# Optimization experiments

Measured on AMD Instinct MI355X. Metric: run time of the kernel, lower is better.

Reference implementation:

```python
import jax, jax.numpy as jnp
import numpy as np

ANNEAL = 0.01  # sigmoid temperature from __init__


def _tsigmoid(x, temp):
    # temperature-controlled sigmoid with the original exponent clamp
    e = jnp.clip(-x / temp, -50.0, 50.0)
    return 1.0 / (1.0 + jnp.exp(e))


def setup_inputs() -> dict:
    key = jax.random.key(0)
    k1, k2 = jax.random.split(key)
    embeddings = jax.random.normal(k1, (384, 512), dtype=jnp.float32)
    labels = jax.random.randint(k2, (384, 40), 0, 2).astype(jnp.int32)
    return {"embeddings": embeddings, "labels": labels}


def reference(embeddings, labels):
    B = embeddings.shape[0]
    # F.normalize(dim=-1) with eps=1e-12
    norm = jnp.maximum(jnp.linalg.norm(embeddings, axis=-1, keepdims=True), 1e-12)
    x = embeddings / norm
    sim = x @ x.T                                   # [B,B] affinity

    # sg[q,j,k] = sigmoid((sim[q,k] - sim[q,j]) / T); diag over (j,k) is exactly 0.5
    sg = _tsigmoid(sim[:, None, :] - sim[:, :, None], ANNEAL)  # [B,B,B]

    # rank over ALL items, excluding k==j (mask = 1-eye): subtract the 0.5 diagonal
    rk_all = 1.0 + sg.sum(-1) - 0.5                 # [B,B]

    pos = labels.astype(sim.dtype).T                # [L,B] binary positive masks
    cnt = pos.sum(-1)                               # [L] positives per label

    # rank among positives of label l: sum over positive k (k != j)
    rk_pos = 1.0 + jnp.einsum('qjk,lk->lqj', sg, pos) - 0.5 * pos[:, None, :]  # [L,B,B]

    # sum over positive (q,j) pairs (including q==j, as in index_select x2)
    pair = pos[:, :, None] * pos[:, None, :]        # [L,B,B]
    s = jnp.sum(pair * (rk_pos / rk_all[None]), axis=(1, 2))  # [L]

    valid = cnt > 1.0                               # labels with >1 positive
    ap = jnp.where(valid, s / jnp.maximum(cnt, 1.0) / B, 0.0)
    n_valid = jnp.maximum(jnp.sum(valid.astype(ap.dtype)), 1.0)
    return jnp.sum((1.0 - ap) * valid.astype(ap.dtype)) / n_valid
```

## Files before the change

kernel.cpp:

```cpp
#include <hip/hip_runtime.h>
#include <hip/hip_bf16.h>
#include <math.h>

#define BN 384
#define DD 512
#define LN 40
#define CLOG 144.26950408889634f

typedef __attribute__((ext_vector_type(8))) short short8;
typedef __attribute__((ext_vector_type(4))) float f32x4;
typedef unsigned short u16;

static __device__ __forceinline__ short bfbits(float f) {
    __hip_bfloat16 h = __float2bfloat16(f);
    return __builtin_bit_cast(short, h);
}

__global__ __launch_bounds__(64) void k_norm(const float* __restrict__ emb,
                                             u16* __restrict__ xh,
                                             u16* __restrict__ xl) {
    int r = blockIdx.x;
    int lane = threadIdx.x;
    const float* row = emb + (size_t)r * DD;
    f32x4 v0 = *(const f32x4*)(row + lane * 8);
    f32x4 v1 = *(const f32x4*)(row + lane * 8 + 4);
    float ss = 0.f;
#pragma unroll
    for (int e = 0; e < 4; ++e) { ss = fmaf(v0[e], v0[e], ss); ss = fmaf(v1[e], v1[e], ss); }
#pragma unroll
    for (int off = 32; off; off >>= 1) ss += __shfl_xor(ss, off);
    float inv = 1.0f / fmaxf(sqrtf(ss), 1e-12f);
    short8 hv, lv;
#pragma unroll
    for (int e = 0; e < 8; ++e) {
        float v = (e < 4 ? v0[e] : v1[e - 4]) * inv;
        __hip_bfloat16 hb = __float2bfloat16(v);
        float hf = __bfloat162float(hb);
        hv[e] = __builtin_bit_cast(short, hb);
        lv[e] = bfbits(v - hf);
    }
    *(short8*)(xh + (size_t)r * DD + lane * 8) = hv;
    *(short8*)(xl + (size_t)r * DD + lane * 8) = lv;
}

__global__ __launch_bounds__(256) void k_meta(const int* __restrict__ labels,
                                              float* __restrict__ w,
                                              float* __restrict__ term0,
                                              u16* __restrict__ pfrag) {
    __shared__ int part[240];
    __shared__ float cnt_s[LN];
    __shared__ float nv_s;
    int tid = threadIdx.x;
    if (tid < 240) {
        int l = tid % LN, seg = tid / LN;
        int c = 0;
        for (int k = seg * 64; k < seg * 64 + 64; ++k) c += labels[k * LN + l];
        part[tid] = c;
    }
    __syncthreads();
    if (tid < LN) {
        int c = 0;
#pragma unroll
        for (int s = 0; s < 6; ++s) c += part[s * LN + tid];
        cnt_s[tid] = (float)c;
    }
    __syncthreads();
    if (tid == 0) {
        float nv = 0.f;
        for (int l = 0; l < LN; ++l) nv += (cnt_s[l] > 1.0f) ? 1.f : 0.f;
        term0[0] = (nv > 0.f) ? 1.0f : 0.0f;
        nv_s = fmaxf(nv, 1.0f);
    }
    __syncthreads();
    if (tid < 48)
        w[tid] = (tid < LN && cnt_s[tid] > 1.0f)
                     ? 1.0f / (cnt_s[tid] * (float)BN * nv_s) : 0.0f;
    for (int u = tid; u < 12 * 3 * 64; u += 256) {
        int ks = u / 192, r = u % 192;
        int lt = r >> 6, ln = r & 63;
        int kb = ks * 32 + ((ln >> 4) << 3);
        short8 vals;
#pragma unroll
        for (int e = 0; e < 8; ++e) {
            int k = kb + e;
            int l = lt * 16 + (ln & 15);
            short bv = 0;
            if (l < LN) bv = labels[k * LN + l] ? (short)0x3F80 : (short)0;
            else if (l == LN) bv = (short)0x3F80;
            vals[e] = bv;
        }
        *(short8*)(pfrag + (size_t)u * 8) = vals;
    }
}

__global__ __launch_bounds__(256) void k_sim(const u16* __restrict__ xh,
                                             const u16* __restrict__ xl,
                                             float* __restrict__ sim) {
    int lane = threadIdx.x & 63;
    int wv = threadIdx.x >> 6;
    int i0 = blockIdx.y * 64 + wv * 16;
    int j0 = blockIdx.x * 64;
    f32x4 acc[4];
#pragma unroll
    for (int jt = 0; jt < 4; ++jt) acc[jt] = (f32x4){0.f, 0.f, 0.f, 0.f};
    int r_i = i0 + (lane & 15);
    for (int ks = 0; ks < DD / 32; ++ks) {
        int kb = ks * 32 + ((lane >> 4) << 3);
        short8 ah = *(const short8*)(xh + (size_t)r_i * DD + kb);
        short8 al = *(const short8*)(xl + (size_t)r_i * DD + kb);
#pragma unroll
        for (int jt = 0; jt < 4; ++jt) {
            int r_j = j0 + jt * 16 + (lane & 15);
            short8 bh = *(const short8*)(xh + (size_t)r_j * DD + kb);
            short8 bl = *(const short8*)(xl + (size_t)r_j * DD + kb);
            acc[jt] = __builtin_amdgcn_mfma_f32_16x16x32_bf16(ah, bh, acc[jt], 0, 0, 0);
            acc[jt] = __builtin_amdgcn_mfma_f32_16x16x32_bf16(ah, bl, acc[jt], 0, 0, 0);
            acc[jt] = __builtin_amdgcn_mfma_f32_16x16x32_bf16(al, bh, acc[jt], 0, 0, 0);
        }
    }
    int rbase = i0 + ((lane >> 4) << 2);
#pragma unroll
    for (int jt = 0; jt < 4; ++jt)
#pragma unroll
        for (int rg = 0; rg < 4; ++rg)
            sim[(size_t)(rbase + rg) * BN + j0 + jt * 16 + (lane & 15)] = acc[jt][rg];
}

__global__ __launch_bounds__(256) void k_main(const float* __restrict__ sim,
                                              const int* __restrict__ labels,
                                              const float* __restrict__ w,
                                              const u16* __restrict__ pfrag,
                                              float* __restrict__ partials) {
    __shared__ float a_lds[BN];
    __shared__ float F_lds[BN];
    __shared__ float wql[48];
    __shared__ float red[16];
    __shared__ float m_sh;
    __shared__ float wpart[4];
    int tid = threadIdx.x;
    int bid = blockIdx.x;
    int q = bid >> 1;
    int lane = tid & 63;
    int wv = tid >> 6;

    float mx = -3.0e38f, mn = 3.0e38f;
    for (int i = tid; i < BN; i += 256) {
        float a = sim[(size_t)q * BN + i] * CLOG;
        a_lds[i] = a;
        mx = fmaxf(mx, a); mn = fminf(mn, a);
    }
#pragma unroll
    for (int off = 32; off; off >>= 1) {
        mx = fmaxf(mx, __shfl_xor(mx, off));
        mn = fminf(mn, __shfl_xor(mn, off));
    }
    if (lane == 0) { red[wv] = mx; red[8 + wv] = mn; }
    __syncthreads();
    if (tid == 0) {
        float M = fmaxf(fmaxf(red[0], red[1]), fmaxf(red[2], red[3]));
        float N = fminf(fminf(red[8], red[9]), fminf(red[10], red[11]));
        m_sh = 0.5f * (M + N);
    }
    if (tid < 48) wql[tid] = (tid < LN) ? w[tid] * (float)labels[q * LN + tid] : 0.0f;
    __syncthreads();
    float m = m_sh;
    for (int i = tid; i < BN; i += 256) {
        float d = fminf(fmaxf(m - a_lds[i], -126.f), 126.f);
        F_lds[i] = __builtin_amdgcn_exp2f(d);
    }
    __syncthreads();

    int jbase = (bid & 1) * 192 + wv * 48;
    float E[3];
#pragma unroll
    for (int t = 0; t < 3; ++t) {
        float aj = a_lds[jbase + t * 16 + (lane & 15)];
        E[t] = __builtin_amdgcn_exp2f(fminf(fmaxf(aj - m, -126.f), 126.f));
    }

    f32x4 acc[3][3];
#pragma unroll
    for (int t = 0; t < 3; ++t)
#pragma unroll
        for (int lt = 0; lt < 3; ++lt) acc[t][lt] = (f32x4){0.f, 0.f, 0.f, 0.f};

    int kg = (lane >> 4) << 3;
    for (int ks = 0; ks < 12; ++ks) {
        const u16* pb = pfrag + ((size_t)(ks * 3) * 64 + lane) * 8;
        short8 bf0 = *(const short8*)(pb);
        short8 bf1 = *(const short8*)(pb + 64 * 8);
        short8 bf2 = *(const short8*)(pb + 128 * 8);
        f32x4 fa = *(const f32x4*)&F_lds[ks * 32 + kg];
        f32x4 fb = *(const f32x4*)&F_lds[ks * 32 + kg + 4];
#pragma unroll
        for (int t = 0; t < 3; ++t) {
            float e = E[t];
            short8 af;
#pragma unroll
            for (int u = 0; u < 4; ++u) {
                float p0 = fmaf(e, fa[u], 1.0f);
                float p1 = fmaf(e, fb[u], 1.0f);
                af[u] = bfbits(__builtin_amdgcn_rcpf(p0));
                af[u + 4] = bfbits(__builtin_amdgcn_rcpf(p1));
            }
            acc[t][0] = __builtin_amdgcn_mfma_f32_16x16x32_bf16(af, bf0, acc[t][0], 0, 0, 0);
            acc[t][1] = __builtin_amdgcn_mfma_f32_16x16x32_bf16(af, bf1, acc[t][1], 0, 0, 0);
            acc[t][2] = __builtin_amdgcn_mfma_f32_16x16x32_bf16(af, bf2, acc[t][2], 0, 0, 0);
        }
    }

    float part = 0.f;
#pragma unroll
    for (int t = 0; t < 3; ++t) {
#pragma unroll
        for (int rg = 0; rg < 4; ++rg) {
            int j = jbase + t * 16 + ((lane >> 4) << 2) + rg;
            float av = __shfl(acc[t][2][rg], (lane & 48) | 8);
            float W = __builtin_amdgcn_rcpf(0.5f + av);
            float sv = 0.f;
#pragma unroll
            for (int lt = 0; lt < 3; ++lt) {
                int l = lt * 16 + (lane & 15);
                float pj = (l < LN) ? (float)labels[j * LN + l] : 0.f;
                sv = fmaf(wql[l] * pj, 0.5f + acc[t][lt][rg], sv);
            }
            part = fmaf(W, sv, part);
        }
    }
#pragma unroll
    for (int off = 32; off; off >>= 1) part += __shfl_xor(part, off);
    if (lane == 0) wpart[wv] = part;
    __syncthreads();
    if (tid == 0) partials[bid] = (wpart[0] + wpart[1]) + (wpart[2] + wpart[3]);
}

__global__ __launch_bounds__(64) void k_final(const float* __restrict__ partials,
                                              const float* __restrict__ term0,
                                              float* __restrict__ out) {
    int lane = threadIdx.x;
    float s = 0.f;
    for (int i = lane; i < 768; i += 64) s += partials[i];
#pragma unroll
    for (int off = 32; off; off >>= 1) s += __shfl_xor(s, off);
    if (lane == 0) out[0] = term0[0] - s;
}

extern "C" void kernel_launch(void* const* d_in, const int* in_sizes, int n_in,
                              void* d_out, int out_size, void* d_ws, size_t ws_size,
                              hipStream_t stream) {
    const float* emb = (const float*)d_in[0];
    const int* labels = (const int*)d_in[1];
    float* out = (float*)d_out;

    char* ws = (char*)d_ws;
    u16* xh      = (u16*)(ws);
    u16* xl      = (u16*)(ws + 393216);
    float* sim   = (float*)(ws + 786432);
    u16* pfrag   = (u16*)(ws + 1376256);
    float* w     = (float*)(ws + 1413120);
    float* term0 = (float*)(ws + 1413312);
    float* parts = (float*)(ws + 1413376);

    k_norm<<<dim3(BN), dim3(64), 0, stream>>>(emb, xh, xl);
    k_meta<<<dim3(1), dim3(256), 0, stream>>>(labels, w, term0, pfrag);
    k_sim<<<dim3(6, 6), dim3(256), 0, stream>>>(xh, xl, sim);
    k_main<<<dim3(BN * 2), dim3(256), 0, stream>>>(sim, labels, w, pfrag, parts);
    k_final<<<dim3(1), dim3(64), 0, stream>>>(parts, term0, out);
}
```

Before: 59.35 us.

## Fuse all stages into one cooperative persistent kernel with grid syncs

Replaces the five separate launches (normalize, label metadata, similarity GEMM, main rank pass, final reduce) with a single cooperative kernel. Stages are separated by grid-wide barriers and work is split across waves and blocks with grid-stride loops. The similarity GEMM is re-tiled to one 16x16 tile per wave, which raises parallelism but drops the reuse of the A fragment across four column tiles. This removes launch gaps and the serial single-block meta kernel, at the cost of grid-sync overhead, an occupancy query on the host for every call, and a limit of 3 blocks per CU.

```diff
diff --git a/kernel.cpp b/kernel.cpp
--- a/kernel.cpp
+++ b/kernel.cpp
@@ -1,6 +1,9 @@
 #include <hip/hip_runtime.h>
 #include <hip/hip_bf16.h>
+#include <hip/hip_cooperative_groups.h>
 #include <math.h>
+
+namespace cg = cooperative_groups;
 
 #define BN 384
 #define DD 512
@@ -16,233 +19,225 @@
     return __builtin_bit_cast(short, h);
 }
 
-__global__ __launch_bounds__(64) void k_norm(const float* __restrict__ emb,
-                                             u16* __restrict__ xh,
-                                             u16* __restrict__ xl) {
-    int r = blockIdx.x;
-    int lane = threadIdx.x;
-    const float* row = emb + (size_t)r * DD;
-    f32x4 v0 = *(const f32x4*)(row + lane * 8);
-    f32x4 v1 = *(const f32x4*)(row + lane * 8 + 4);
-    float ss = 0.f;
-#pragma unroll
-    for (int e = 0; e < 4; ++e) { ss = fmaf(v0[e], v0[e], ss); ss = fmaf(v1[e], v1[e], ss); }
-#pragma unroll
-    for (int off = 32; off; off >>= 1) ss += __shfl_xor(ss, off);
-    float inv = 1.0f / fmaxf(sqrtf(ss), 1e-12f);
-    short8 hv, lv;
-#pragma unroll
-    for (int e = 0; e < 8; ++e) {
-        float v = (e < 4 ? v0[e] : v1[e - 4]) * inv;
-        __hip_bfloat16 hb = __float2bfloat16(v);
-        float hf = __bfloat162float(hb);
-        hv[e] = __builtin_bit_cast(short, hb);
-        lv[e] = bfbits(v - hf);
-    }
-    *(short8*)(xh + (size_t)r * DD + lane * 8) = hv;
-    *(short8*)(xl + (size_t)r * DD + lane * 8) = lv;
-}
-
-__global__ __launch_bounds__(256) void k_meta(const int* __restrict__ labels,
-                                              float* __restrict__ w,
-                                              float* __restrict__ term0,
-                                              u16* __restrict__ pfrag) {
-    __shared__ int part[240];
-    __shared__ float cnt_s[LN];
-    __shared__ float nv_s;
+__global__ __launch_bounds__(256, 3) void k_fused(const float* __restrict__ emb,
+                                                  const int* __restrict__ labels,
+                                                  float* __restrict__ out,
+                                                  void* __restrict__ wsv) {
+    u16* xh = (u16*)wsv;
+    u16* xl = xh + BN * DD;
+    float* sim = (float*)(xl + BN * DD);
+    u16* pfrag = (u16*)(sim + BN * BN);
+    float* cnt = (float*)(pfrag + 36 * 64 * 8);
+    float* w = cnt + 64;
+    float* term0 = w + 64;
+    float* partials = term0 + 64;
+
+    cg::grid_group gg = cg::this_grid();
+    int bid = blockIdx.x;
     int tid = threadIdx.x;
-    if (tid < 240) {
-        int l = tid % LN, seg = tid / LN;
-        int c = 0;
-        for (int k = seg * 64; k < seg * 64 + 64; ++k) c += labels[k * LN + l];
-        part[tid] = c;
-    }
-    __syncthreads();
-    if (tid < LN) {
-        int c = 0;
-#pragma unroll
-        for (int s = 0; s < 6; ++s) c += part[s * LN + tid];
-        cnt_s[tid] = (float)c;
-    }
-    __syncthreads();
-    if (tid == 0) {
-        float nv = 0.f;
-        for (int l = 0; l < LN; ++l) nv += (cnt_s[l] > 1.0f) ? 1.f : 0.f;
-        term0[0] = (nv > 0.f) ? 1.0f : 0.0f;
-        nv_s = fmaxf(nv, 1.0f);
-    }
-    __syncthreads();
-    if (tid < 48)
-        w[tid] = (tid < LN && cnt_s[tid] > 1.0f)
-                     ? 1.0f / (cnt_s[tid] * (float)BN * nv_s) : 0.0f;
-    for (int u = tid; u < 12 * 3 * 64; u += 256) {
-        int ks = u / 192, r = u % 192;
-        int lt = r >> 6, ln = r & 63;
-        int kb = ks * 32 + ((ln >> 4) << 3);
-        short8 vals;
-#pragma unroll
-        for (int e = 0; e < 8; ++e) {
-            int k = kb + e;
-            int l = lt * 16 + (ln & 15);
-            short bv = 0;
-            if (l < LN) bv = labels[k * LN + l] ? (short)0x3F80 : (short)0;
-            else if (l == LN) bv = (short)0x3F80;
-            vals[e] = bv;
-        }
-        *(short8*)(pfrag + (size_t)u * 8) = vals;
-    }
-}
-
-__global__ __launch_bounds__(256) void k_sim(const u16* __restrict__ xh,
-                                             const u16* __restrict__ xl,
-                                             float* __restrict__ sim) {
-    int lane = threadIdx.x & 63;
-    int wv = threadIdx.x >> 6;
-    int i0 = blockIdx.y * 64 + wv * 16;
-    int j0 = blockIdx.x * 64;
-    f32x4 acc[4];
-#pragma unroll
-    for (int jt = 0; jt < 4; ++jt) acc[jt] = (f32x4){0.f, 0.f, 0.f, 0.f};
-    int r_i = i0 + (lane & 15);
-    for (int ks = 0; ks < DD / 32; ++ks) {
-        int kb = ks * 32 + ((lane >> 4) << 3);
-        short8 ah = *(const short8*)(xh + (size_t)r_i * DD + kb);
-        short8 al = *(const short8*)(xl + (size_t)r_i * DD + kb);
-#pragma unroll
-        for (int jt = 0; jt < 4; ++jt) {
-            int r_j = j0 + jt * 16 + (lane & 15);
-            short8 bh = *(const short8*)(xh + (size_t)r_j * DD + kb);
-            short8 bl = *(const short8*)(xl + (size_t)r_j * DD + kb);
-            acc[jt] = __builtin_amdgcn_mfma_f32_16x16x32_bf16(ah, bh, acc[jt], 0, 0, 0);
-            acc[jt] = __builtin_amdgcn_mfma_f32_16x16x32_bf16(ah, bl, acc[jt], 0, 0, 0);
-            acc[jt] = __builtin_amdgcn_mfma_f32_16x16x32_bf16(al, bh, acc[jt], 0, 0, 0);
-        }
-    }
-    int rbase = i0 + ((lane >> 4) << 2);
-#pragma unroll
-    for (int jt = 0; jt < 4; ++jt)
-#pragma unroll
-        for (int rg = 0; rg < 4; ++rg)
-            sim[(size_t)(rbase + rg) * BN + j0 + jt * 16 + (lane & 15)] = acc[jt][rg];
-}
-
-__global__ __launch_bounds__(256) void k_main(const float* __restrict__ sim,
-                                              const int* __restrict__ labels,
-                                              const float* __restrict__ w,
-                                              const u16* __restrict__ pfrag,
-                                              float* __restrict__ partials) {
+    int lane = tid & 63;
+    int wv = tid >> 6;
+    int nwg = gridDim.x;
+    int nwaves = nwg * 4;
+    int gw = bid * 4 + wv;
+
     __shared__ float a_lds[BN];
     __shared__ float F_lds[BN];
     __shared__ float wql[48];
     __shared__ float red[16];
     __shared__ float m_sh;
     __shared__ float wpart[4];
-    int tid = threadIdx.x;
-    int bid = blockIdx.x;
-    int q = bid >> 1;
-    int lane = tid & 63;
-    int wv = tid >> 6;
-
-    float mx = -3.0e38f, mn = 3.0e38f;
-    for (int i = tid; i < BN; i += 256) {
-        float a = sim[(size_t)q * BN + i] * CLOG;
-        a_lds[i] = a;
-        mx = fmaxf(mx, a); mn = fminf(mn, a);
-    }
-#pragma unroll
-    for (int off = 32; off; off >>= 1) {
-        mx = fmaxf(mx, __shfl_xor(mx, off));
-        mn = fminf(mn, __shfl_xor(mn, off));
-    }
-    if (lane == 0) { red[wv] = mx; red[8 + wv] = mn; }
-    __syncthreads();
-    if (tid == 0) {
-        float M = fmaxf(fmaxf(red[0], red[1]), fmaxf(red[2], red[3]));
-        float N = fminf(fminf(red[8], red[9]), fminf(red[10], red[11]));
-        m_sh = 0.5f * (M + N);
-    }
-    if (tid < 48) wql[tid] = (tid < LN) ? w[tid] * (float)labels[q * LN + tid] : 0.0f;
-    __syncthreads();
-    float m = m_sh;
-    for (int i = tid; i < BN; i += 256) {
-        float d = fminf(fmaxf(m - a_lds[i], -126.f), 126.f);
-        F_lds[i] = __builtin_amdgcn_exp2f(d);
-    }
-    __syncthreads();
-
-    int jbase = (bid & 1) * 192 + wv * 48;
-    float E[3];
-#pragma unroll
-    for (int t = 0; t < 3; ++t) {
-        float aj = a_lds[jbase + t * 16 + (lane & 15)];
-        E[t] = __builtin_amdgcn_exp2f(fminf(fmaxf(aj - m, -126.f), 126.f));
-    }
-
-    f32x4 acc[3][3];
-#pragma unroll
-    for (int t = 0; t < 3; ++t)
-#pragma unroll
-        for (int lt = 0; lt < 3; ++lt) acc[t][lt] = (f32x4){0.f, 0.f, 0.f, 0.f};
-
-    int kg = (lane >> 4) << 3;
-    for (int ks = 0; ks < 12; ++ks) {
-        const u16* pb = pfrag + ((size_t)(ks * 3) * 64 + lane) * 8;
-        short8 bf0 = *(const short8*)(pb);
-        short8 bf1 = *(const short8*)(pb + 64 * 8);
-        short8 bf2 = *(const short8*)(pb + 128 * 8);
-        f32x4 fa = *(const f32x4*)&F_lds[ks * 32 + kg];
-        f32x4 fb = *(const f32x4*)&F_lds[ks * 32 + kg + 4];
+
+    for (int t = gw; t < 436; t += nwaves) {
+        if (t < BN) {
+            const float* row = emb + (size_t)t * DD;
+            f32x4 v0 = *(const f32x4*)(row + lane * 8);
+            f32x4 v1 = *(const f32x4*)(row + lane * 8 + 4);
+            float ss = 0.f;
+#pragma unroll
+            for (int e = 0; e < 4; ++e) { ss = fmaf(v0[e], v0[e], ss); ss = fmaf(v1[e], v1[e], ss); }
+#pragma unroll
+            for (int off = 32; off; off >>= 1) ss += __shfl_xor(ss, off);
+            float inv = 1.0f / fmaxf(sqrtf(ss), 1e-12f);
+            short8 hv, lv;
+#pragma unroll
+            for (int e = 0; e < 8; ++e) {
+                float v = (e < 4 ? v0[e] : v1[e - 4]) * inv;
+                __hip_bfloat16 hb = __float2bfloat16(v);
+                float hf = __bfloat162float(hb);
+                hv[e] = __builtin_bit_cast(short, hb);
+                lv[e] = bfbits(v - hf);
+            }
+            *(short8*)(xh + (size_t)t * DD + lane * 8) = hv;
+            *(short8*)(xl + (size_t)t * DD + lane * 8) = lv;
+        } else if (t < 424) {
+            int l = t - BN;
+            int c = 0;
+#pragma unroll
+            for (int k = lane; k < BN; k += 64) c += labels[k * LN + l];
+#pragma unroll
+            for (int off = 32; off; off >>= 1) c += __shfl_xor(c, off);
+            if (lane == 0) cnt[l] = (float)c;
+        } else {
+            int ks = t - 424;
+#pragma unroll
+            for (int lt = 0; lt < 3; ++lt) {
+                int u = (ks * 3 + lt) * 64 + lane;
+                int kb = ks * 32 + ((lane >> 4) << 3);
+                short8 vals;
+#pragma unroll
+                for (int e = 0; e < 8; ++e) {
+                    int k = kb + e;
+                    int l = lt * 16 + (lane & 15);
+                    short bv = 0;
+                    if (l < LN) bv = labels[k * LN + l] ? (short)0x3F80 : (short)0;
+                    else if (l == LN) bv = (short)0x3F80;
+                    vals[e] = bv;
+                }
+                *(short8*)(pfrag + (size_t)u * 8) = vals;
+            }
+        }
+    }
+    gg.sync();
+
+    for (int t = gw; t < 577; t += nwaves) {
+        if (t < 576) {
+            int i0 = (t / 24) * 16;
+            int j0 = (t % 24) * 16;
+            f32x4 acc = (f32x4){0.f, 0.f, 0.f, 0.f};
+            int r_i = i0 + (lane & 15);
+            int r_j = j0 + (lane & 15);
+#pragma unroll
+            for (int ks = 0; ks < DD / 32; ++ks) {
+                int kb = ks * 32 + ((lane >> 4) << 3);
+                short8 ah = *(const short8*)(xh + (size_t)r_i * DD + kb);
+                short8 al = *(const short8*)(xl + (size_t)r_i * DD + kb);
+                short8 bh = *(const short8*)(xh + (size_t)r_j * DD + kb);
+                short8 bl = *(const short8*)(xl + (size_t)r_j * DD + kb);
+                acc = __builtin_amdgcn_mfma_f32_16x16x32_bf16(ah, bh, acc, 0, 0, 0);
+                acc = __builtin_amdgcn_mfma_f32_16x16x32_bf16(ah, bl, acc, 0, 0, 0);
+                acc = __builtin_amdgcn_mfma_f32_16x16x32_bf16(al, bh, acc, 0, 0, 0);
+            }
+            int rbase = i0 + ((lane >> 4) << 2);
+#pragma unroll
+            for (int rg = 0; rg < 4; ++rg)
+                sim[(size_t)(rbase + rg) * BN + j0 + (lane & 15)] = acc[rg];
+        } else {
+            float c = (lane < LN) ? cnt[lane] : 0.f;
+            bool valid = (lane < LN) && (c > 1.0f);
+            unsigned long long bal = __ballot(valid);
+            float nv = (float)__popcll(bal);
+            float nvm = fmaxf(nv, 1.0f);
+            if (lane < 48) w[lane] = valid ? 1.0f / (c * (float)BN * nvm) : 0.0f;
+            if (lane == 0) term0[0] = (nv > 0.f) ? 1.0f : 0.0f;
+        }
+    }
+    gg.sync();
+
+    for (int task = bid; task < 2 * BN; task += nwg) {
+        int q = task >> 1;
+        float mx = -3.0e38f, mn = 3.0e38f;
+        for (int i = tid; i < BN; i += 256) {
+            float a = sim[(size_t)q * BN + i] * CLOG;
+            a_lds[i] = a;
+            mx = fmaxf(mx, a); mn = fminf(mn, a);
+        }
+#pragma unroll
+        for (int off = 32; off; off >>= 1) {
+            mx = fmaxf(mx, __shfl_xor(mx, off));
+            mn = fminf(mn, __shfl_xor(mn, off));
+        }
+        if (lane == 0) { red[wv] = mx; red[8 + wv] = mn; }
+        __syncthreads();
+        if (tid == 0) {
+            float M = fmaxf(fmaxf(red[0], red[1]), fmaxf(red[2], red[3]));
+            float N = fminf(fminf(red[8], red[9]), fminf(red[10], red[11]));
+            m_sh = 0.5f * (M + N);
+        }
+        if (tid < 48) wql[tid] = (tid < LN) ? w[tid] * (float)labels[q * LN + tid] : 0.0f;
+        __syncthreads();
+        float m = m_sh;
+        for (int i = tid; i < BN; i += 256) {
+            float d = fminf(fmaxf(m - a_lds[i], -126.f), 126.f);
+            F_lds[i] = __builtin_amdgcn_exp2f(d);
+        }
+        __syncthreads();
+
+        int jbase = (task & 1) * 192 + wv * 48;
+        float E[3];
 #pragma unroll
         for (int t = 0; t < 3; ++t) {
-            float e = E[t];
-            short8 af;
-#pragma unroll
-            for (int u = 0; u < 4; ++u) {
-                float p0 = fmaf(e, fa[u], 1.0f);
-                float p1 = fmaf(e, fb[u], 1.0f);
-                af[u] = bfbits(__builtin_amdgcn_rcpf(p0));
-                af[u + 4] = bfbits(__builtin_amdgcn_rcpf(p1));
-            }
-            acc[t][0] = __builtin_amdgcn_mfma_f32_16x16x32_bf16(af, bf0, acc[t][0], 0, 0, 0);
-            acc[t][1] = __builtin_amdgcn_mfma_f32_16x16x32_bf16(af, bf1, acc[t][1], 0, 0, 0);
-            acc[t][2] = __builtin_amdgcn_mfma_f32_16x16x32_bf16(af, bf2, acc[t][2], 0, 0, 0);
-        }
-    }
-
-    float part = 0.f;
-#pragma unroll
-    for (int t = 0; t < 3; ++t) {
-#pragma unroll
-        for (int rg = 0; rg < 4; ++rg) {
-            int j = jbase + t * 16 + ((lane >> 4) << 2) + rg;
-            float av = __shfl(acc[t][2][rg], (lane & 48) | 8);
-            float W = __builtin_amdgcn_rcpf(0.5f + av);
-            float sv = 0.f;
-#pragma unroll
-            for (int lt = 0; lt < 3; ++lt) {
-                int l = lt * 16 + (lane & 15);
-                float pj = (l < LN) ? (float)labels[j * LN + l] : 0.f;
-                sv = fmaf(wql[l] * pj, 0.5f + acc[t][lt][rg], sv);
-            }
-            part = fmaf(W, sv, part);
-        }
-    }
-#pragma unroll
-    for (int off = 32; off; off >>= 1) part += __shfl_xor(part, off);
-    if (lane == 0) wpart[wv] = part;
-    __syncthreads();
-    if (tid == 0) partials[bid] = (wpart[0] + wpart[1]) + (wpart[2] + wpart[3]);
-}
-
-__global__ __launch_bounds__(64) void k_final(const float* __restrict__ partials,
-                                              const float* __restrict__ term0,
-                                              float* __restrict__ out) {
-    int lane = threadIdx.x;
-    float s = 0.f;
-    for (int i = lane; i < 768; i += 64) s += partials[i];
-#pragma unroll
-    for (int off = 32; off; off >>= 1) s += __shfl_xor(s, off);
-    if (lane == 0) out[0] = term0[0] - s;
+            float aj = a_lds[jbase + t * 16 + (lane & 15)];
+            E[t] = __builtin_amdgcn_exp2f(fminf(fmaxf(aj - m, -126.f), 126.f));
+        }
+
+        f32x4 acc[3][3];
+#pragma unroll
+        for (int t = 0; t < 3; ++t)
+#pragma unroll
+            for (int lt = 0; lt < 3; ++lt) acc[t][lt] = (f32x4){0.f, 0.f, 0.f, 0.f};
+
+        int kg = (lane >> 4) << 3;
+        for (int ks = 0; ks < 12; ++ks) {
+            const u16* pb = pfrag + ((size_t)(ks * 3) * 64 + lane) * 8;
+            short8 bf0 = *(const short8*)(pb);
+            short8 bf1 = *(const short8*)(pb + 64 * 8);
+            short8 bf2 = *(const short8*)(pb + 128 * 8);
+            f32x4 fa = *(const f32x4*)&F_lds[ks * 32 + kg];
+            f32x4 fb = *(const f32x4*)&F_lds[ks * 32 + kg + 4];
+#pragma unroll
+            for (int t = 0; t < 3; ++t) {
+                float e = E[t];
+                short8 af;
+#pragma unroll
+                for (int u = 0; u < 4; ++u) {
+                    float p0 = fmaf(e, fa[u], 1.0f);
+                    float p1 = fmaf(e, fb[u], 1.0f);
+                    af[u] = bfbits(__builtin_amdgcn_rcpf(p0));
+                    af[u + 4] = bfbits(__builtin_amdgcn_rcpf(p1));
+                }
+                acc[t][0] = __builtin_amdgcn_mfma_f32_16x16x32_bf16(af, bf0, acc[t][0], 0, 0, 0);
+                acc[t][1] = __builtin_amdgcn_mfma_f32_16x16x32_bf16(af, bf1, acc[t][1], 0, 0, 0);
+                acc[t][2] = __builtin_amdgcn_mfma_f32_16x16x32_bf16(af, bf2, acc[t][2], 0, 0, 0);
+            }
+        }
+
+        float part = 0.f;
+#pragma unroll
+        for (int t = 0; t < 3; ++t) {
+#pragma unroll
+            for (int rg = 0; rg < 4; ++rg) {
+                int j = jbase + t * 16 + ((lane >> 4) << 2) + rg;
+                float av = __shfl(acc[t][2][rg], (lane & 48) | 8);
+                float W = __builtin_amdgcn_rcpf(0.5f + av);
+                float sv = 0.f;
+#pragma unroll
+                for (int lt = 0; lt < 3; ++lt) {
+                    int l = lt * 16 + (lane & 15);
+                    float pj = (l < LN) ? (float)labels[j * LN + l] : 0.f;
+                    sv = fmaf(wql[l] * pj, 0.5f + acc[t][lt][rg], sv);
+                }
+                part = fmaf(W, sv, part);
+            }
+        }
+#pragma unroll
+        for (int off = 32; off; off >>= 1) part += __shfl_xor(part, off);
+        if (lane == 0) wpart[wv] = part;
+        __syncthreads();
+        if (tid == 0) partials[task] = (wpart[0] + wpart[1]) + (wpart[2] + wpart[3]);
+        __syncthreads();
+    }
+    gg.sync();
+
+    if (bid == 0) {
+        float s = 0.f;
+        for (int i = tid; i < 768; i += 256) s += partials[i];
+#pragma unroll
+        for (int off = 32; off; off >>= 1) s += __shfl_xor(s, off);
+        if (lane == 0) red[wv] = s;
+        __syncthreads();
+        if (tid == 0) out[0] = term0[0] - ((red[0] + red[1]) + (red[2] + red[3]));
+    }
 }
 
 extern "C" void kernel_launch(void* const* d_in, const int* in_sizes, int n_in,
@@ -251,19 +246,15 @@
     const float* emb = (const float*)d_in[0];
     const int* labels = (const int*)d_in[1];
     float* out = (float*)d_out;
-
-    char* ws = (char*)d_ws;
-    u16* xh      = (u16*)(ws);
-    u16* xl      = (u16*)(ws + 393216);
-    float* sim   = (float*)(ws + 786432);
-    u16* pfrag   = (u16*)(ws + 1376256);
-    float* w     = (float*)(ws + 1413120);
-    float* term0 = (float*)(ws + 1413312);
-    float* parts = (float*)(ws + 1413376);
-
-    k_norm<<<dim3(BN), dim3(64), 0, stream>>>(emb, xh, xl);
-    k_meta<<<dim3(1), dim3(256), 0, stream>>>(labels, w, term0, pfrag);
-    k_sim<<<dim3(6, 6), dim3(256), 0, stream>>>(xh, xl, sim);
-    k_main<<<dim3(BN * 2), dim3(256), 0, stream>>>(sim, labels, w, pfrag, parts);
-    k_final<<<dim3(1), dim3(64), 0, stream>>>(parts, term0, out);
+    void* ws = d_ws;
+
+    int maxb = 0;
+    hipOccupancyMaxActiveBlocksPerMultiprocessor(&maxb, k_fused, 256, 0);
+    if (maxb < 1) maxb = 1;
+    long grid = (long)maxb * 256;
+    if (grid > 768) grid = 768;
+
+    void* args[] = {(void*)&emb, (void*)&labels, (void*)&out, (void*)&ws};
+    hipLaunchCooperativeKernel((const void*)k_fused, dim3((unsigned)grid), dim3(256),
+                               args, 0, stream);
 }
```

After: 138.6 us. +133.5%, slower.
